# Performance work log

Measured on AMD Instinct MI355X. Metric: run time of the kernel, lower is better.

## Reference

```python
import jax, jax.numpy as jnp
import numpy as np

N_ITEMS = 7000
N_USERS = 30000
N_NODES = N_ITEMS + N_USERS  # 37000
D = 128        # embed_dim == user_embed_dim
E = 400000     # num edges
R = 10         # n_relation (num ratings)
NB = 8         # num_bases
B = 512        # batch of conversations
L = 100        # max context items per sample


def setup_inputs() -> dict:
    key = jax.random.key(0)
    ks = jax.random.split(key, 16)
    # edges: item (source) -> user (target), disjoint id ranges as in load_data
    src = jax.random.randint(ks[0], (E,), 0, N_ITEMS)
    dst = jax.random.randint(ks[1], (E,), N_ITEMS, N_NODES)
    edge_index = jnp.stack([src, dst]).astype(jnp.int64)
    edge_type = jax.random.randint(ks[2], (E,), 0, R).astype(jnp.int64)

    def make_ctx(k1, k2):
        c = jax.random.randint(k1, (B, L), 0, N_ITEMS)
        drop = jax.random.uniform(k2, (B, L)) < 0.3  # -1 padding as in batch lists
        return jnp.where(drop, -1, c).astype(jnp.int64)

    ctx_init = make_ctx(ks[3], ks[4])
    ctx_resp = make_ctx(ks[5], ks[6])

    s = 0.02
    basis = jax.random.normal(ks[7], (NB, N_NODES, D), jnp.float32) * s
    comp = jax.random.normal(ks[8], (R, NB), jnp.float32) * s
    root = jax.random.normal(ks[9], (N_NODES, D), jnp.float32) * s
    bias = jnp.zeros((D,), jnp.float32)
    attn_a = jax.random.normal(ks[10], (D, D), jnp.float32) * s
    attn_b = jax.random.normal(ks[11], (D,), jnp.float32) * s
    fc1_w = jax.random.normal(ks[12], (D, D), jnp.float32) * s
    fc1_b = jnp.zeros((D,), jnp.float32)
    fc2_w = jax.random.normal(ks[13], (D, D), jnp.float32) * s
    fc2_b = jnp.zeros((D,), jnp.float32)
    efc1_w = jax.random.normal(ks[14], (2 * D, D), jnp.float32) * s
    efc1_b = jnp.zeros((D,), jnp.float32)
    efc2_w = jax.random.normal(ks[15], (D, D), jnp.float32) * s
    efc2_b = jnp.zeros((D,), jnp.float32)
    return dict(edge_index=edge_index, edge_type=edge_type, ctx_init=ctx_init,
                ctx_resp=ctx_resp, basis=basis, comp=comp, root=root, bias=bias,
                attn_a=attn_a, attn_b=attn_b, fc1_w=fc1_w, fc1_b=fc1_b,
                fc2_w=fc2_w, fc2_b=fc2_b, efc1_w=efc1_w, efc1_b=efc1_b,
                efc2_w=efc2_w, efc2_b=efc2_b)


def _rgcn(basis, comp, root, bias, edge_index, edge_type):
    # RGCNConv with x=None: per-edge message W_{r_e}[src_e], mean-aggregated
    # per (target, relation), summed over relations, plus root lookup + bias.
    src, dst = edge_index[0], edge_index[1]
    nb, n, d = basis.shape
    r = comp.shape[0]
    cpe = comp[edge_type]  # [E, NB]
    msg = jnp.zeros((src.shape[0], d), basis.dtype)
    for b in range(nb):  # small fixed basis count; avoids [E,NB,D] gather
        msg = msg + cpe[:, b:b + 1] * basis[b][src]
    seg = dst * r + edge_type  # per-(node, relation) segment for mean aggr
    sums = jax.ops.segment_sum(msg, seg, num_segments=n * r).reshape(n, r, d)
    cnt = jax.ops.segment_sum(jnp.ones_like(edge_type, basis.dtype), seg,
                              num_segments=n * r).reshape(n, r, 1)
    return root + bias + (sums / jnp.maximum(cnt, 1.0)).sum(axis=1)  # [N, D]


def _item_user_means(node_emb, edge_index):
    # mean over users connected to each item (edge_idx[1][edge_idx[0]==item])
    src, dst = edge_index[0], edge_index[1]
    isum = jax.ops.segment_sum(node_emb[dst], src, num_segments=N_ITEMS)
    icnt = jax.ops.segment_sum(jnp.ones_like(src, node_emb.dtype), src,
                               num_segments=N_ITEMS)
    item_mean = isum / jnp.maximum(icnt, 1.0)[:, None]  # [N_ITEMS, D]
    return item_mean, icnt > 0


def _attn_pool(ctx, item_mean, item_has_users, attn_a, attn_b):
    # SelfAttentionBatch over each sample's item reps (padding/-1 & degree-0
    # items masked out; all-empty samples -> zeros, as in original).
    valid = ctx >= 0
    idx = jnp.clip(ctx, 0, N_ITEMS - 1)
    h = item_mean[idx]                       # [B, L, D]
    valid = valid & item_has_users[idx]
    e = jnp.einsum('bld,d->bl', jnp.tanh(jnp.einsum('bld,de->ble', h, attn_a)),
                   attn_b)
    attn = jax.nn.softmax(jnp.where(valid, e, -1e9), axis=-1)
    attn = jnp.where(valid, attn, 0.0)
    return jnp.einsum('bl,bld->bd', attn, h)  # [B, D]


def _project(x, w1, b1, w2, b2):
    # fc1 -> relu -> fc2 -> relu (as in _project_user_interaction_*)
    return jax.nn.relu(jax.nn.relu(x @ w1 + b1) @ w2 + b2)


def reference(edge_index, edge_type, ctx_init, ctx_resp, basis, comp, root,
              bias, attn_a, attn_b, fc1_w, fc1_b, fc2_w, fc2_b, efc1_w,
              efc1_b, efc2_w, efc2_b):
    node_emb = _rgcn(basis, comp, root, bias, edge_index, edge_type)
    item_mean, item_has = _item_user_means(node_emb, edge_index)
    p_init = _project(_attn_pool(ctx_init, item_mean, item_has, attn_a, attn_b),
                      fc1_w, fc1_b, fc2_w, fc2_b)
    p_resp = _project(_attn_pool(ctx_resp, item_mean, item_has, attn_a, attn_b),
                      fc1_w, fc1_b, fc2_w, fc2_b)
    both = jnp.concatenate([p_init, p_resp], axis=1)  # [B, 2D]
    profile = _project(both, efc1_w, efc1_b, efc2_w, efc2_b)  # [B, D]
    return profile, p_init, p_resp
```

## Files before the change

### kernel.cpp

```cpp
#include <hip/hip_runtime.h>
#include <math.h>

typedef unsigned int uint;

#define N_ITEMS 7000
#define N_NODES 37000
#define N_USERS 30000
#define DIM     128
#define HD      64
#define NREL    10
#define NBASES  8
#define BATCH   512
#define CTXL    100
#define E_MAX   400000

#define OFF_CNT    0
#define OFF_ICNT   (OFF_CNT + N_USERS * NREL)
#define OFF_UCNT   (OFF_ICNT + N_ITEMS)
#define ZERO_ELEMS (OFF_UCNT + N_USERS)
#define OFF_ICUR   ZERO_ELEMS
#define OFF_UCUR   (OFF_ICUR + N_ITEMS)
#define OFF_ICSR   (OFF_UCUR + N_USERS)
#define OFF_UCSR   (OFF_ICSR + E_MAX)
#define OFF_WC     (OFF_UCSR + E_MAX)
#define OFF_ACC    (OFF_WC + NREL * N_ITEMS * HD)
#define OFF_MEAN   (OFF_ACC + N_USERS * HD)
#define OFF_SCORE  (OFF_MEAN + N_ITEMS * HD)

__device__ __forceinline__ float2 bf2f(uint p) {
  float2 r;
  r.x = __uint_as_float(p << 16);
  r.y = __uint_as_float(p & 0xffff0000u);
  return r;
}
__device__ __forceinline__ uint f2bf(float x, float y) {
  uint a = __float_as_uint(x), b = __float_as_uint(y);
  a += 0x7fffu + ((a >> 16) & 1u);
  b += 0x7fffu + ((b >> 16) & 1u);
  return (a >> 16) | (b & 0xffff0000u);
}

__device__ __forceinline__ float wave_sum(float v) {
#pragma unroll
  for (int o = 1; o < 64; o <<= 1) v += __shfl_xor(v, o, 64);
  return v;
}
__device__ __forceinline__ float wave_max(float v) {
#pragma unroll
  for (int o = 1; o < 64; o <<= 1) v = fmaxf(v, __shfl_xor(v, o, 64));
  return v;
}

__global__ __launch_bounds__(HD) void k_combine(const float* __restrict__ basis,
                                                const float* __restrict__ comp,
                                                uint* __restrict__ Wc) {
  int i = blockIdx.x, t = threadIdx.x;
  float2 bb[NBASES];
#pragma unroll
  for (int b = 0; b < NBASES; ++b)
    bb[b] = ((const float2*)(basis + ((size_t)b * N_NODES + i) * DIM))[t];
#pragma unroll
  for (int r = 0; r < NREL; ++r) {
    float sx = 0.f, sy = 0.f;
#pragma unroll
    for (int b = 0; b < NBASES; ++b) {
      float c = comp[r * NBASES + b];
      sx = fmaf(c, bb[b].x, sx);
      sy = fmaf(c, bb[b].y, sy);
    }
    Wc[((size_t)r * N_ITEMS + i) * HD + t] = f2bf(sx, sy);
  }
}

__global__ __launch_bounds__(256) void k_count(const int* __restrict__ ei,
                                               const int* __restrict__ et, int E,
                                               int* __restrict__ cnt,
                                               int* __restrict__ icnt,
                                               int* __restrict__ ucnt) {
  int e = blockIdx.x * 256 + threadIdx.x;
  if (e >= E) return;
  int s = ei[e];
  int u0 = ei[E + e] - N_ITEMS;
  int t = et[e];
  atomicAdd(&cnt[u0 * NREL + t], 1);
  atomicAdd(&icnt[s], 1);
  atomicAdd(&ucnt[u0], 1);
}

__global__ __launch_bounds__(1024) void k_scan(const int* __restrict__ icnt,
                                               const int* __restrict__ ucnt,
                                               int* __restrict__ icur,
                                               int* __restrict__ ucur) {
  __shared__ int ss[1024];
  const int* in;
  int n;
  int* cur;
  if (blockIdx.x == 0) { in = icnt; n = N_ITEMS; cur = icur; }
  else                 { in = ucnt; n = N_USERS; cur = ucur; }
  int t = threadIdx.x;
  int chunk = (n + 1023) / 1024;
  int lo = t * chunk, hi = lo + chunk;
  if (lo > n) lo = n;
  if (hi > n) hi = n;
  int s = 0;
  for (int i = lo; i < hi; ++i) s += in[i];
  ss[t] = s;
  __syncthreads();
  for (int o = 1; o < 1024; o <<= 1) {
    int v = (t >= o) ? ss[t - o] : 0;
    __syncthreads();
    ss[t] += v;
    __syncthreads();
  }
  int base = (t > 0) ? ss[t - 1] : 0;
  for (int i = lo; i < hi; ++i) { cur[i] = base; base += in[i]; }
}

__global__ __launch_bounds__(256) void k_fill(const int* __restrict__ ei,
                                              const int* __restrict__ et, int E,
                                              int* __restrict__ icur,
                                              int* __restrict__ ucur,
                                              int* __restrict__ icsr,
                                              int* __restrict__ ucsr) {
  int e = blockIdx.x * 256 + threadIdx.x;
  if (e >= E) return;
  int s = ei[e];
  int u0 = ei[E + e] - N_ITEMS;
  int t = et[e];
  icsr[atomicAdd(&icur[s], 1)] = u0;
  ucsr[atomicAdd(&ucur[u0], 1)] = s | (t << 16);
}

__global__ __launch_bounds__(HD) void k_useragg(const int* __restrict__ ucnt,
                                                const int* __restrict__ ucur,
                                                const int* __restrict__ ucsr,
                                                const int* __restrict__ cnt,
                                                const uint* __restrict__ Wc,
                                                const float* __restrict__ root,
                                                uint* __restrict__ acc) {
  __shared__ float wrow[NREL];
  __shared__ int sedge[HD];
  int u = blockIdx.x, t = threadIdx.x;
  if (t < NREL) {
    int c = cnt[u * NREL + t];
    wrow[t] = (c > 0) ? 1.0f / (float)c : 0.0f;
  }
  int deg = ucnt[u];
  int base = ucur[u] - deg;
  float2 a0 = {0.f, 0.f}, a1 = {0.f, 0.f}, a2 = {0.f, 0.f}, a3 = {0.f, 0.f};
  for (int j0 = 0; j0 < deg; j0 += HD) {
    int m = deg - j0;
    if (m > HD) m = HD;
    __syncthreads();
    if (t < m) sedge[t] = ucsr[base + j0 + t];
    __syncthreads();
    int j = 0;
    for (; j + 4 <= m; j += 4) {
      int p0 = sedge[j], p1 = sedge[j + 1], p2 = sedge[j + 2], p3 = sedge[j + 3];
      uint q0 = Wc[(size_t)((p0 >> 16) * N_ITEMS + (p0 & 0xffff)) * HD + t];
      uint q1 = Wc[(size_t)((p1 >> 16) * N_ITEMS + (p1 & 0xffff)) * HD + t];
      uint q2 = Wc[(size_t)((p2 >> 16) * N_ITEMS + (p2 & 0xffff)) * HD + t];
      uint q3 = Wc[(size_t)((p3 >> 16) * N_ITEMS + (p3 & 0xffff)) * HD + t];
      float w0 = wrow[p0 >> 16], w1 = wrow[p1 >> 16];
      float w2 = wrow[p2 >> 16], w3 = wrow[p3 >> 16];
      float2 f0 = bf2f(q0), f1 = bf2f(q1), f2 = bf2f(q2), f3 = bf2f(q3);
      a0.x = fmaf(w0, f0.x, a0.x); a0.y = fmaf(w0, f0.y, a0.y);
      a1.x = fmaf(w1, f1.x, a1.x); a1.y = fmaf(w1, f1.y, a1.y);
      a2.x = fmaf(w2, f2.x, a2.x); a2.y = fmaf(w2, f2.y, a2.y);
      a3.x = fmaf(w3, f3.x, a3.x); a3.y = fmaf(w3, f3.y, a3.y);
    }
    for (; j < m; ++j) {
      int p = sedge[j];
      uint q = Wc[(size_t)((p >> 16) * N_ITEMS + (p & 0xffff)) * HD + t];
      float w = wrow[p >> 16];
      float2 f = bf2f(q);
      a0.x = fmaf(w, f.x, a0.x); a0.y = fmaf(w, f.y, a0.y);
    }
  }
  float2 r = ((const float2*)(root + (size_t)(N_ITEMS + u) * DIM))[t];
  r.x += a0.x + a1.x + a2.x + a3.x;
  r.y += a0.y + a1.y + a2.y + a3.y;
  acc[(size_t)u * HD + t] = f2bf(r.x, r.y);
}

__global__ __launch_bounds__(HD) void k_itemagg(const int* __restrict__ icnt,
                                                const int* __restrict__ icur,
                                                const int* __restrict__ icsr,
                                                const uint* __restrict__ acc,
                                                const float* __restrict__ bias,
                                                const float* __restrict__ attn_a,
                                                const float* __restrict__ attn_b,
                                                uint* __restrict__ mean,
                                                float* __restrict__ score) {
  __shared__ int sedge[HD];
  __shared__ float sm[DIM];
  int i = blockIdx.x, t = threadIdx.x;
  int deg = icnt[i];
  int base = icur[i] - deg;
  float2 a0 = {0.f, 0.f}, a1 = {0.f, 0.f}, a2 = {0.f, 0.f}, a3 = {0.f, 0.f};
  for (int j0 = 0; j0 < deg; j0 += HD) {
    int m = deg - j0;
    if (m > HD) m = HD;
    __syncthreads();
    if (t < m) sedge[t] = icsr[base + j0 + t];
    __syncthreads();
    int j = 0;
    for (; j + 4 <= m; j += 4) {
      uint q0 = acc[(size_t)sedge[j] * HD + t];
      uint q1 = acc[(size_t)sedge[j + 1] * HD + t];
      uint q2 = acc[(size_t)sedge[j + 2] * HD + t];
      uint q3 = acc[(size_t)sedge[j + 3] * HD + t];
      float2 f0 = bf2f(q0), f1 = bf2f(q1), f2 = bf2f(q2), f3 = bf2f(q3);
      a0.x += f0.x; a0.y += f0.y;
      a1.x += f1.x; a1.y += f1.y;
      a2.x += f2.x; a2.y += f2.y;
      a3.x += f3.x; a3.y += f3.y;
    }
    for (; j < m; ++j) {
      float2 f = bf2f(acc[(size_t)sedge[j] * HD + t]);
      a0.x += f.x; a0.y += f.y;
    }
  }
  float2 mv = {0.f, 0.f};
  if (deg > 0) {
    float inv = 1.0f / (float)deg;
    float2 bvec = ((const float2*)bias)[t];
    mv.x = (a0.x + a1.x + a2.x + a3.x) * inv + bvec.x;
    mv.y = (a0.y + a1.y + a2.y + a3.y) * inv + bvec.y;
  }
  mean[(size_t)i * HD + t] = f2bf(mv.x, mv.y);
  sm[2 * t] = mv.x;
  sm[2 * t + 1] = mv.y;
  __syncthreads();
  float z0 = 0.f, z1 = 0.f;
#pragma unroll 8
  for (int k = 0; k < DIM; ++k) {
    float2 w = ((const float2*)(attn_a + (size_t)k * DIM))[t];
    float h = sm[k];
    z0 = fmaf(h, w.x, z0);
    z1 = fmaf(h, w.y, z1);
  }
  float2 ab = ((const float2*)attn_b)[t];
  float v = wave_sum(tanhf(z0) * ab.x + tanhf(z1) * ab.y);
  if (t == 0) score[i] = (deg > 0) ? v : -1e9f;
}

__global__ __launch_bounds__(HD) void k_pool(const int* __restrict__ ctx0,
                                             const int* __restrict__ ctx1,
                                             const uint* __restrict__ mean,
                                             const float* __restrict__ score,
                                             const float* __restrict__ fc1_w,
                                             const float* __restrict__ fc1_b,
                                             const float* __restrict__ fc2_w,
                                             const float* __restrict__ fc2_b,
                                             float* __restrict__ out) {
  __shared__ float shw[CTXL];
  __shared__ int shi[CTXL];
  __shared__ float shv[DIM];
  int b = blockIdx.x & (BATCH - 1);
  int c = blockIdx.x >> 9;
  int t = threadIdx.x;
  const int* cx = (c == 0 ? ctx0 : ctx1) + (size_t)b * CTXL;

  int id0 = cx[t];
  float e0 = (id0 >= 0) ? score[id0] : -1e9f;
  int id1 = -1;
  float e1 = -3.0e38f;
  if (t + HD < CTXL) {
    id1 = cx[t + HD];
    e1 = (id1 >= 0) ? score[id1] : -1e9f;
  }
  float m = wave_max(fmaxf(e0, e1));
  float x0 = expf(e0 - m);
  float x1 = (t + HD < CTXL) ? expf(e1 - m) : 0.f;
  float inv = 1.0f / wave_sum(x0 + x1);
  shw[t] = (id0 >= 0) ? x0 * inv : 0.f;
  shi[t] = (id0 >= 0) ? id0 : 0;
  if (t + HD < CTXL) {
    shw[t + HD] = (id1 >= 0) ? x1 * inv : 0.f;
    shi[t + HD] = (id1 >= 0) ? id1 : 0;
  }
  __syncthreads();

  float2 a0 = {0.f, 0.f}, a1 = {0.f, 0.f}, a2 = {0.f, 0.f}, a3 = {0.f, 0.f};
#pragma unroll 5
  for (int l = 0; l < CTXL; l += 4) {
    float w0 = shw[l], w1 = shw[l + 1], w2 = shw[l + 2], w3 = shw[l + 3];
    uint q0 = mean[(size_t)shi[l] * HD + t];
    uint q1 = mean[(size_t)shi[l + 1] * HD + t];
    uint q2 = mean[(size_t)shi[l + 2] * HD + t];
    uint q3 = mean[(size_t)shi[l + 3] * HD + t];
    float2 f0 = bf2f(q0), f1 = bf2f(q1), f2 = bf2f(q2), f3 = bf2f(q3);
    a0.x = fmaf(w0, f0.x, a0.x); a0.y = fmaf(w0, f0.y, a0.y);
    a1.x = fmaf(w1, f1.x, a1.x); a1.y = fmaf(w1, f1.y, a1.y);
    a2.x = fmaf(w2, f2.x, a2.x); a2.y = fmaf(w2, f2.y, a2.y);
    a3.x = fmaf(w3, f3.x, a3.x); a3.y = fmaf(w3, f3.y, a3.y);
  }
  __syncthreads();
  shv[2 * t] = a0.x + a1.x + a2.x + a3.x;
  shv[2 * t + 1] = a0.y + a1.y + a2.y + a3.y;
  __syncthreads();

  float2 z = ((const float2*)fc1_b)[t];
#pragma unroll 8
  for (int k = 0; k < DIM; ++k) {
    float2 w = ((const float2*)(fc1_w + (size_t)k * DIM))[t];
    float h = shv[k];
    z.x = fmaf(h, w.x, z.x);
    z.y = fmaf(h, w.y, z.y);
  }
  z.x = fmaxf(z.x, 0.f);
  z.y = fmaxf(z.y, 0.f);
  __syncthreads();
  shv[2 * t] = z.x;
  shv[2 * t + 1] = z.y;
  __syncthreads();

  float2 z2 = ((const float2*)fc2_b)[t];
#pragma unroll 8
  for (int k = 0; k < DIM; ++k) {
    float2 w = ((const float2*)(fc2_w + (size_t)k * DIM))[t];
    float h = shv[k];
    z2.x = fmaf(h, w.x, z2.x);
    z2.y = fmaf(h, w.y, z2.y);
  }
  z2.x = fmaxf(z2.x, 0.f);
  z2.y = fmaxf(z2.y, 0.f);
  ((float2*)(out + (size_t)(1 + c) * BATCH * DIM + (size_t)b * DIM))[t] = z2;
}

__global__ __launch_bounds__(HD) void k_profile(const float* __restrict__ efc1_w,
                                                const float* __restrict__ efc1_b,
                                                const float* __restrict__ efc2_w,
                                                const float* __restrict__ efc2_b,
                                                float* __restrict__ out) {
  __shared__ float shv[2 * DIM];
  __shared__ float sh2[DIM];
  int b = blockIdx.x, t = threadIdx.x;
  float2 p0 = ((const float2*)(out + (size_t)BATCH * DIM + (size_t)b * DIM))[t];
  float2 p1 = ((const float2*)(out + (size_t)2 * BATCH * DIM + (size_t)b * DIM))[t];
  shv[2 * t] = p0.x;
  shv[2 * t + 1] = p0.y;
  shv[DIM + 2 * t] = p1.x;
  shv[DIM + 2 * t + 1] = p1.y;
  __syncthreads();
  float2 z = ((const float2*)efc1_b)[t];
#pragma unroll 8
  for (int k = 0; k < 2 * DIM; ++k) {
    float2 w = ((const float2*)(efc1_w + (size_t)k * DIM))[t];
    float h = shv[k];
    z.x = fmaf(h, w.x, z.x);
    z.y = fmaf(h, w.y, z.y);
  }
  z.x = fmaxf(z.x, 0.f);
  z.y = fmaxf(z.y, 0.f);
  __syncthreads();
  sh2[2 * t] = z.x;
  sh2[2 * t + 1] = z.y;
  __syncthreads();
  float2 z2 = ((const float2*)efc2_b)[t];
#pragma unroll 8
  for (int k = 0; k < DIM; ++k) {
    float2 w = ((const float2*)(efc2_w + (size_t)k * DIM))[t];
    float h = sh2[k];
    z2.x = fmaf(h, w.x, z2.x);
    z2.y = fmaf(h, w.y, z2.y);
  }
  z2.x = fmaxf(z2.x, 0.f);
  z2.y = fmaxf(z2.y, 0.f);
  ((float2*)(out + (size_t)b * DIM))[t] = z2;
}

extern "C" void kernel_launch(void* const* d_in, const int* in_sizes, int n_in,
                              void* d_out, int out_size, void* d_ws, size_t ws_size,
                              hipStream_t stream) {
  const int*   ei     = (const int*)d_in[0];
  const int*   et     = (const int*)d_in[1];
  const int*   ctx0   = (const int*)d_in[2];
  const int*   ctx1   = (const int*)d_in[3];
  const float* basis  = (const float*)d_in[4];
  const float* comp   = (const float*)d_in[5];
  const float* root   = (const float*)d_in[6];
  const float* bias   = (const float*)d_in[7];
  const float* attn_a = (const float*)d_in[8];
  const float* attn_b = (const float*)d_in[9];
  const float* fc1_w  = (const float*)d_in[10];
  const float* fc1_b  = (const float*)d_in[11];
  const float* fc2_w  = (const float*)d_in[12];
  const float* fc2_b  = (const float*)d_in[13];
  const float* efc1_w = (const float*)d_in[14];
  const float* efc1_b = (const float*)d_in[15];
  const float* efc2_w = (const float*)d_in[16];
  const float* efc2_b = (const float*)d_in[17];
  float* out = (float*)d_out;

  const int E = in_sizes[1];

  float* ws   = (float*)d_ws;
  int*  cnt   = (int*)(ws + OFF_CNT);
  int*  icnt  = (int*)(ws + OFF_ICNT);
  int*  ucnt  = (int*)(ws + OFF_UCNT);
  int*  icur  = (int*)(ws + OFF_ICUR);
  int*  ucur  = (int*)(ws + OFF_UCUR);
  int*  icsr  = (int*)(ws + OFF_ICSR);
  int*  ucsr  = (int*)(ws + OFF_UCSR);
  uint* Wc    = (uint*)(ws + OFF_WC);
  uint* acc   = (uint*)(ws + OFF_ACC);
  uint* mean  = (uint*)(ws + OFF_MEAN);
  float* score = ws + OFF_SCORE;

  hipMemsetAsync(d_ws, 0, (size_t)ZERO_ELEMS * sizeof(float), stream);

  k_combine<<<N_ITEMS, HD, 0, stream>>>(basis, comp, Wc);
  k_count<<<(E + 255) / 256, 256, 0, stream>>>(ei, et, E, cnt, icnt, ucnt);
  k_scan<<<2, 1024, 0, stream>>>(icnt, ucnt, icur, ucur);
  k_fill<<<(E + 255) / 256, 256, 0, stream>>>(ei, et, E, icur, ucur, icsr, ucsr);
  k_useragg<<<N_USERS, HD, 0, stream>>>(ucnt, ucur, ucsr, cnt, Wc, root, acc);
  k_itemagg<<<N_ITEMS, HD, 0, stream>>>(icnt, icur, icsr, acc, bias, attn_a, attn_b,
                                        mean, score);
  k_pool<<<2 * BATCH, HD, 0, stream>>>(ctx0, ctx1, mean, score, fc1_w, fc1_b,
                                       fc2_w, fc2_b, out);
  k_profile<<<BATCH, HD, 0, stream>>>(efc1_w, efc1_b, efc2_w, efc2_b, out);
}
```

Baseline: 481.3 us.

## Fuse combine/count and pool/profile kernels, use wave shuffles instead of LDS

Merges the basis-combine and edge-count kernels into one launch, and the pooling and profile kernels into one 128-thread block per batch row. The user and item aggregation kernels now broadcast edge indices and relation weights through wave shuffles instead of shared memory with barriers. They also unroll 16 gathers per step into 8 accumulators to keep more loads in flight. This cuts launch count, barriers and LDS traffic, at the cost of more registers and some gathers that are issued and then masked out on partial chunks.

```diff
diff --git a/kernel.cpp b/kernel.cpp
--- a/kernel.cpp
+++ b/kernel.cpp
@@ -51,40 +51,45 @@
   return v;
 }
 
-__global__ __launch_bounds__(HD) void k_combine(const float* __restrict__ basis,
-                                                const float* __restrict__ comp,
-                                                uint* __restrict__ Wc) {
-  int i = blockIdx.x, t = threadIdx.x;
-  float2 bb[NBASES];
-#pragma unroll
-  for (int b = 0; b < NBASES; ++b)
-    bb[b] = ((const float2*)(basis + ((size_t)b * N_NODES + i) * DIM))[t];
-#pragma unroll
-  for (int r = 0; r < NREL; ++r) {
-    float sx = 0.f, sy = 0.f;
-#pragma unroll
-    for (int b = 0; b < NBASES; ++b) {
-      float c = comp[r * NBASES + b];
-      sx = fmaf(c, bb[b].x, sx);
-      sy = fmaf(c, bb[b].y, sy);
-    }
-    Wc[((size_t)r * N_ITEMS + i) * HD + t] = f2bf(sx, sy);
-  }
-}
-
-__global__ __launch_bounds__(256) void k_count(const int* __restrict__ ei,
-                                               const int* __restrict__ et, int E,
-                                               int* __restrict__ cnt,
-                                               int* __restrict__ icnt,
-                                               int* __restrict__ ucnt) {
-  int e = blockIdx.x * 256 + threadIdx.x;
-  if (e >= E) return;
-  int s = ei[e];
-  int u0 = ei[E + e] - N_ITEMS;
-  int t = et[e];
-  atomicAdd(&cnt[u0 * NREL + t], 1);
-  atomicAdd(&icnt[s], 1);
-  atomicAdd(&ucnt[u0], 1);
+#define COMBINE_BLOCKS (N_ITEMS / 4)
+__global__ __launch_bounds__(256) void k_initcomb(const float* __restrict__ basis,
+                                                  const float* __restrict__ comp,
+                                                  uint* __restrict__ Wc,
+                                                  const int* __restrict__ ei,
+                                                  const int* __restrict__ et, int E,
+                                                  int* __restrict__ cnt,
+                                                  int* __restrict__ icnt,
+                                                  int* __restrict__ ucnt) {
+  int tid = threadIdx.x;
+  if (blockIdx.x < COMBINE_BLOCKS) {
+    int i = blockIdx.x * 4 + (tid >> 6);
+    int lane = tid & 63;
+    float2 bb[NBASES];
+#pragma unroll
+    for (int b = 0; b < NBASES; ++b)
+      bb[b] = ((const float2*)basis)[((size_t)b * N_NODES + i) * HD + lane];
+#pragma unroll
+    for (int r = 0; r < NREL; ++r) {
+      float sx = 0.f, sy = 0.f;
+#pragma unroll
+      for (int b = 0; b < NBASES; ++b) {
+        float c = comp[r * NBASES + b];
+        sx = fmaf(c, bb[b].x, sx);
+        sy = fmaf(c, bb[b].y, sy);
+      }
+      Wc[((size_t)r * N_ITEMS + i) * HD + lane] = f2bf(sx, sy);
+    }
+  } else {
+    int e = (blockIdx.x - COMBINE_BLOCKS) * 256 + tid;
+    if (e < E) {
+      int s  = ei[e];
+      int u0 = ei[E + e] - N_ITEMS;
+      int t  = et[e];
+      atomicAdd(&cnt[u0 * NREL + t], 1);
+      atomicAdd(&icnt[s], 1);
+      atomicAdd(&ucnt[u0], 1);
+    }
+  }
 }
 
 __global__ __launch_bounds__(1024) void k_scan(const int* __restrict__ icnt,
@@ -131,59 +136,51 @@
   ucsr[atomicAdd(&ucur[u0], 1)] = s | (t << 16);
 }
 
-__global__ __launch_bounds__(HD) void k_useragg(const int* __restrict__ ucnt,
+__global__ __launch_bounds__(64) void k_useragg(const int* __restrict__ ucnt,
                                                 const int* __restrict__ ucur,
                                                 const int* __restrict__ ucsr,
                                                 const int* __restrict__ cnt,
                                                 const uint* __restrict__ Wc,
                                                 const float* __restrict__ root,
                                                 uint* __restrict__ acc) {
-  __shared__ float wrow[NREL];
-  __shared__ int sedge[HD];
-  int u = blockIdx.x, t = threadIdx.x;
-  if (t < NREL) {
-    int c = cnt[u * NREL + t];
-    wrow[t] = (c > 0) ? 1.0f / (float)c : 0.0f;
-  }
+  int u = blockIdx.x, lane = threadIdx.x;
   int deg = ucnt[u];
   int base = ucur[u] - deg;
-  float2 a0 = {0.f, 0.f}, a1 = {0.f, 0.f}, a2 = {0.f, 0.f}, a3 = {0.f, 0.f};
-  for (int j0 = 0; j0 < deg; j0 += HD) {
+  float wl = 0.f;
+  if (lane < NREL) {
+    int c = cnt[u * NREL + lane];
+    wl = (c > 0) ? 1.0f / (float)c : 0.0f;
+  }
+  float2 av[8];
+#pragma unroll
+  for (int k = 0; k < 8; ++k) { av[k].x = 0.f; av[k].y = 0.f; }
+  for (int j0 = 0; j0 < deg; j0 += 64) {
     int m = deg - j0;
-    if (m > HD) m = HD;
-    __syncthreads();
-    if (t < m) sedge[t] = ucsr[base + j0 + t];
-    __syncthreads();
-    int j = 0;
-    for (; j + 4 <= m; j += 4) {
-      int p0 = sedge[j], p1 = sedge[j + 1], p2 = sedge[j + 2], p3 = sedge[j + 3];
-      uint q0 = Wc[(size_t)((p0 >> 16) * N_ITEMS + (p0 & 0xffff)) * HD + t];
-      uint q1 = Wc[(size_t)((p1 >> 16) * N_ITEMS + (p1 & 0xffff)) * HD + t];
-      uint q2 = Wc[(size_t)((p2 >> 16) * N_ITEMS + (p2 & 0xffff)) * HD + t];
-      uint q3 = Wc[(size_t)((p3 >> 16) * N_ITEMS + (p3 & 0xffff)) * HD + t];
-      float w0 = wrow[p0 >> 16], w1 = wrow[p1 >> 16];
-      float w2 = wrow[p2 >> 16], w3 = wrow[p3 >> 16];
-      float2 f0 = bf2f(q0), f1 = bf2f(q1), f2 = bf2f(q2), f3 = bf2f(q3);
-      a0.x = fmaf(w0, f0.x, a0.x); a0.y = fmaf(w0, f0.y, a0.y);
-      a1.x = fmaf(w1, f1.x, a1.x); a1.y = fmaf(w1, f1.y, a1.y);
-      a2.x = fmaf(w2, f2.x, a2.x); a2.y = fmaf(w2, f2.y, a2.y);
-      a3.x = fmaf(w3, f3.x, a3.x); a3.y = fmaf(w3, f3.y, a3.y);
-    }
-    for (; j < m; ++j) {
-      int p = sedge[j];
-      uint q = Wc[(size_t)((p >> 16) * N_ITEMS + (p & 0xffff)) * HD + t];
-      float w = wrow[p >> 16];
-      float2 f = bf2f(q);
-      a0.x = fmaf(w, f.x, a0.x); a0.y = fmaf(w, f.y, a0.y);
-    }
-  }
-  float2 r = ((const float2*)(root + (size_t)(N_ITEMS + u) * DIM))[t];
-  r.x += a0.x + a1.x + a2.x + a3.x;
-  r.y += a0.y + a1.y + a2.y + a3.y;
-  acc[(size_t)u * HD + t] = f2bf(r.x, r.y);
-}
-
-__global__ __launch_bounds__(HD) void k_itemagg(const int* __restrict__ icnt,
+    if (m > 64) m = 64;
+    int pl = (lane < m) ? ucsr[base + j0 + lane] : 0;
+    for (int kk = 0; kk < m; kk += 16) {
+#pragma unroll
+      for (int k = 0; k < 16; ++k) {
+        int idx = kk + k;
+        int p = __shfl(pl, idx & 63);
+        int r = p >> 16;
+        float w = (idx < m) ? __shfl(wl, r) : 0.f;
+        uint q = Wc[(size_t)(r * N_ITEMS + (p & 0xffff)) * HD + lane];
+        float2 f = bf2f(q);
+        av[k & 7].x = fmaf(w, f.x, av[k & 7].x);
+        av[k & 7].y = fmaf(w, f.y, av[k & 7].y);
+      }
+    }
+  }
+  float2 rt = ((const float2*)root)[(size_t)(N_ITEMS + u) * HD + lane];
+  rt.x += ((av[0].x + av[1].x) + (av[2].x + av[3].x)) +
+          ((av[4].x + av[5].x) + (av[6].x + av[7].x));
+  rt.y += ((av[0].y + av[1].y) + (av[2].y + av[3].y)) +
+          ((av[4].y + av[5].y) + (av[6].y + av[7].y));
+  acc[(size_t)u * HD + lane] = f2bf(rt.x, rt.y);
+}
+
+__global__ __launch_bounds__(64) void k_itemagg(const int* __restrict__ icnt,
                                                 const int* __restrict__ icur,
                                                 const int* __restrict__ icsr,
                                                 const uint* __restrict__ acc,
@@ -192,183 +189,189 @@
                                                 const float* __restrict__ attn_b,
                                                 uint* __restrict__ mean,
                                                 float* __restrict__ score) {
-  __shared__ int sedge[HD];
-  __shared__ float sm[DIM];
-  int i = blockIdx.x, t = threadIdx.x;
+  int i = blockIdx.x, lane = threadIdx.x;
   int deg = icnt[i];
   int base = icur[i] - deg;
-  float2 a0 = {0.f, 0.f}, a1 = {0.f, 0.f}, a2 = {0.f, 0.f}, a3 = {0.f, 0.f};
-  for (int j0 = 0; j0 < deg; j0 += HD) {
+  float2 av[8];
+#pragma unroll
+  for (int k = 0; k < 8; ++k) { av[k].x = 0.f; av[k].y = 0.f; }
+  for (int j0 = 0; j0 < deg; j0 += 64) {
     int m = deg - j0;
-    if (m > HD) m = HD;
-    __syncthreads();
-    if (t < m) sedge[t] = icsr[base + j0 + t];
-    __syncthreads();
-    int j = 0;
-    for (; j + 4 <= m; j += 4) {
-      uint q0 = acc[(size_t)sedge[j] * HD + t];
-      uint q1 = acc[(size_t)sedge[j + 1] * HD + t];
-      uint q2 = acc[(size_t)sedge[j + 2] * HD + t];
-      uint q3 = acc[(size_t)sedge[j + 3] * HD + t];
-      float2 f0 = bf2f(q0), f1 = bf2f(q1), f2 = bf2f(q2), f3 = bf2f(q3);
-      a0.x += f0.x; a0.y += f0.y;
-      a1.x += f1.x; a1.y += f1.y;
-      a2.x += f2.x; a2.y += f2.y;
-      a3.x += f3.x; a3.y += f3.y;
-    }
-    for (; j < m; ++j) {
-      float2 f = bf2f(acc[(size_t)sedge[j] * HD + t]);
-      a0.x += f.x; a0.y += f.y;
-    }
-  }
+    if (m > 64) m = 64;
+    int pl = (lane < m) ? icsr[base + j0 + lane] : 0;
+    for (int kk = 0; kk < m; kk += 16) {
+#pragma unroll
+      for (int k = 0; k < 16; ++k) {
+        int idx = kk + k;
+        int u0 = __shfl(pl, idx & 63);
+        uint q = acc[(size_t)u0 * HD + lane];
+        float2 f = bf2f(q);
+        if (idx < m) {
+          av[k & 7].x += f.x;
+          av[k & 7].y += f.y;
+        }
+      }
+    }
+  }
+  float sx = ((av[0].x + av[1].x) + (av[2].x + av[3].x)) +
+             ((av[4].x + av[5].x) + (av[6].x + av[7].x));
+  float sy = ((av[0].y + av[1].y) + (av[2].y + av[3].y)) +
+             ((av[4].y + av[5].y) + (av[6].y + av[7].y));
   float2 mv = {0.f, 0.f};
   if (deg > 0) {
     float inv = 1.0f / (float)deg;
-    float2 bvec = ((const float2*)bias)[t];
-    mv.x = (a0.x + a1.x + a2.x + a3.x) * inv + bvec.x;
-    mv.y = (a0.y + a1.y + a2.y + a3.y) * inv + bvec.y;
-  }
-  mean[(size_t)i * HD + t] = f2bf(mv.x, mv.y);
-  sm[2 * t] = mv.x;
-  sm[2 * t + 1] = mv.y;
-  __syncthreads();
+    float2 bv = ((const float2*)bias)[lane];
+    mv.x = sx * inv + bv.x;
+    mv.y = sy * inv + bv.y;
+  }
+  mean[(size_t)i * HD + lane] = f2bf(mv.x, mv.y);
   float z0 = 0.f, z1 = 0.f;
 #pragma unroll 8
-  for (int k = 0; k < DIM; ++k) {
-    float2 w = ((const float2*)(attn_a + (size_t)k * DIM))[t];
-    float h = sm[k];
-    z0 = fmaf(h, w.x, z0);
-    z1 = fmaf(h, w.y, z1);
-  }
-  float2 ab = ((const float2*)attn_b)[t];
+  for (int k2 = 0; k2 < HD; ++k2) {
+    float hx = __shfl(mv.x, k2);
+    float hy = __shfl(mv.y, k2);
+    float2 w0 = ((const float2*)attn_a)[(size_t)(2 * k2) * HD + lane];
+    float2 w1 = ((const float2*)attn_a)[(size_t)(2 * k2 + 1) * HD + lane];
+    z0 = fmaf(hx, w0.x, z0); z1 = fmaf(hx, w0.y, z1);
+    z0 = fmaf(hy, w1.x, z0); z1 = fmaf(hy, w1.y, z1);
+  }
+  float2 ab = ((const float2*)attn_b)[lane];
   float v = wave_sum(tanhf(z0) * ab.x + tanhf(z1) * ab.y);
-  if (t == 0) score[i] = (deg > 0) ? v : -1e9f;
-}
-
-__global__ __launch_bounds__(HD) void k_pool(const int* __restrict__ ctx0,
-                                             const int* __restrict__ ctx1,
-                                             const uint* __restrict__ mean,
-                                             const float* __restrict__ score,
-                                             const float* __restrict__ fc1_w,
-                                             const float* __restrict__ fc1_b,
-                                             const float* __restrict__ fc2_w,
-                                             const float* __restrict__ fc2_b,
-                                             float* __restrict__ out) {
-  __shared__ float shw[CTXL];
-  __shared__ int shi[CTXL];
-  __shared__ float shv[DIM];
-  int b = blockIdx.x & (BATCH - 1);
-  int c = blockIdx.x >> 9;
-  int t = threadIdx.x;
-  const int* cx = (c == 0 ? ctx0 : ctx1) + (size_t)b * CTXL;
-
-  int id0 = cx[t];
-  float e0 = (id0 >= 0) ? score[id0] : -1e9f;
-  int id1 = -1;
-  float e1 = -3.0e38f;
-  if (t + HD < CTXL) {
-    id1 = cx[t + HD];
-    e1 = (id1 >= 0) ? score[id1] : -1e9f;
-  }
-  float m = wave_max(fmaxf(e0, e1));
-  float x0 = expf(e0 - m);
-  float x1 = (t + HD < CTXL) ? expf(e1 - m) : 0.f;
-  float inv = 1.0f / wave_sum(x0 + x1);
-  shw[t] = (id0 >= 0) ? x0 * inv : 0.f;
-  shi[t] = (id0 >= 0) ? id0 : 0;
-  if (t + HD < CTXL) {
-    shw[t + HD] = (id1 >= 0) ? x1 * inv : 0.f;
-    shi[t + HD] = (id1 >= 0) ? id1 : 0;
-  }
-  __syncthreads();
-
-  float2 a0 = {0.f, 0.f}, a1 = {0.f, 0.f}, a2 = {0.f, 0.f}, a3 = {0.f, 0.f};
-#pragma unroll 5
-  for (int l = 0; l < CTXL; l += 4) {
-    float w0 = shw[l], w1 = shw[l + 1], w2 = shw[l + 2], w3 = shw[l + 3];
-    uint q0 = mean[(size_t)shi[l] * HD + t];
-    uint q1 = mean[(size_t)shi[l + 1] * HD + t];
-    uint q2 = mean[(size_t)shi[l + 2] * HD + t];
-    uint q3 = mean[(size_t)shi[l + 3] * HD + t];
-    float2 f0 = bf2f(q0), f1 = bf2f(q1), f2 = bf2f(q2), f3 = bf2f(q3);
-    a0.x = fmaf(w0, f0.x, a0.x); a0.y = fmaf(w0, f0.y, a0.y);
-    a1.x = fmaf(w1, f1.x, a1.x); a1.y = fmaf(w1, f1.y, a1.y);
-    a2.x = fmaf(w2, f2.x, a2.x); a2.y = fmaf(w2, f2.y, a2.y);
-    a3.x = fmaf(w3, f3.x, a3.x); a3.y = fmaf(w3, f3.y, a3.y);
-  }
-  __syncthreads();
-  shv[2 * t] = a0.x + a1.x + a2.x + a3.x;
-  shv[2 * t + 1] = a0.y + a1.y + a2.y + a3.y;
-  __syncthreads();
-
-  float2 z = ((const float2*)fc1_b)[t];
-#pragma unroll 8
-  for (int k = 0; k < DIM; ++k) {
-    float2 w = ((const float2*)(fc1_w + (size_t)k * DIM))[t];
-    float h = shv[k];
-    z.x = fmaf(h, w.x, z.x);
-    z.y = fmaf(h, w.y, z.y);
-  }
-  z.x = fmaxf(z.x, 0.f);
-  z.y = fmaxf(z.y, 0.f);
-  __syncthreads();
-  shv[2 * t] = z.x;
-  shv[2 * t + 1] = z.y;
-  __syncthreads();
-
-  float2 z2 = ((const float2*)fc2_b)[t];
-#pragma unroll 8
-  for (int k = 0; k < DIM; ++k) {
-    float2 w = ((const float2*)(fc2_w + (size_t)k * DIM))[t];
-    float h = shv[k];
-    z2.x = fmaf(h, w.x, z2.x);
-    z2.y = fmaf(h, w.y, z2.y);
-  }
-  z2.x = fmaxf(z2.x, 0.f);
-  z2.y = fmaxf(z2.y, 0.f);
-  ((float2*)(out + (size_t)(1 + c) * BATCH * DIM + (size_t)b * DIM))[t] = z2;
-}
-
-__global__ __launch_bounds__(HD) void k_profile(const float* __restrict__ efc1_w,
+  if (lane == 0) score[i] = (deg > 0) ? v : -1e9f;
+}
+
+__global__ __launch_bounds__(128) void k_batch2(const int* __restrict__ ctx0,
+                                                const int* __restrict__ ctx1,
+                                                const uint* __restrict__ mean,
+                                                const float* __restrict__ score,
+                                                const float* __restrict__ fc1_w,
+                                                const float* __restrict__ fc1_b,
+                                                const float* __restrict__ fc2_w,
+                                                const float* __restrict__ fc2_b,
+                                                const float* __restrict__ efc1_w,
                                                 const float* __restrict__ efc1_b,
                                                 const float* __restrict__ efc2_w,
                                                 const float* __restrict__ efc2_b,
                                                 float* __restrict__ out) {
-  __shared__ float shv[2 * DIM];
-  __shared__ float sh2[DIM];
-  int b = blockIdx.x, t = threadIdx.x;
-  float2 p0 = ((const float2*)(out + (size_t)BATCH * DIM + (size_t)b * DIM))[t];
-  float2 p1 = ((const float2*)(out + (size_t)2 * BATCH * DIM + (size_t)b * DIM))[t];
-  shv[2 * t] = p0.x;
-  shv[2 * t + 1] = p0.y;
-  shv[DIM + 2 * t] = p1.x;
-  shv[DIM + 2 * t + 1] = p1.y;
-  __syncthreads();
-  float2 z = ((const float2*)efc1_b)[t];
-#pragma unroll 8
-  for (int k = 0; k < 2 * DIM; ++k) {
-    float2 w = ((const float2*)(efc1_w + (size_t)k * DIM))[t];
-    float h = shv[k];
-    z.x = fmaf(h, w.x, z.x);
-    z.y = fmaf(h, w.y, z.y);
+  __shared__ float2 shp[2][HD];
+  int b = blockIdx.x;
+  int wv = threadIdx.x >> 6;
+  int lane = threadIdx.x & 63;
+  float2* out2 = (float2*)out;
+
+  const int* cx = (wv ? ctx1 : ctx0) + (size_t)b * CTXL;
+  int id0 = cx[lane];
+  float e0 = (id0 >= 0) ? score[id0] : -1e9f;
+  int id1 = -1;
+  float e1 = -3.0e38f;
+  if (lane < CTXL - 64) {
+    id1 = cx[64 + lane];
+    e1 = (id1 >= 0) ? score[id1] : -1e9f;
+  }
+  float mx = wave_max(fmaxf(e0, e1));
+  float x0 = expf(e0 - mx);
+  float x1 = (lane < CTXL - 64) ? expf(e1 - mx) : 0.f;
+  float inv = 1.0f / wave_sum(x0 + x1);
+  float w0 = (id0 >= 0) ? x0 * inv : 0.f;
+  float w1 = (id1 >= 0) ? x1 * inv : 0.f;
+  int i0 = (id0 >= 0) ? id0 : 0;
+  int i1 = (id1 >= 0) ? id1 : 0;
+
+  float2 av[4];
+#pragma unroll
+  for (int k = 0; k < 4; ++k) { av[k].x = 0.f; av[k].y = 0.f; }
+  for (int j = 0; j < 64; j += 4) {
+#pragma unroll
+    for (int k = 0; k < 4; ++k) {
+      int ii = __shfl(i0, j + k);
+      float ww = __shfl(w0, j + k);
+      float2 f = bf2f(mean[(size_t)ii * HD + lane]);
+      av[k].x = fmaf(ww, f.x, av[k].x);
+      av[k].y = fmaf(ww, f.y, av[k].y);
+    }
+  }
+  for (int j = 0; j < CTXL - 64; j += 4) {
+#pragma unroll
+    for (int k = 0; k < 4; ++k) {
+      int ii = __shfl(i1, j + k);
+      float ww = __shfl(w1, j + k);
+      float2 f = bf2f(mean[(size_t)ii * HD + lane]);
+      av[k].x = fmaf(ww, f.x, av[k].x);
+      av[k].y = fmaf(ww, f.y, av[k].y);
+    }
+  }
+  float2 pool;
+  pool.x = (av[0].x + av[1].x) + (av[2].x + av[3].x);
+  pool.y = (av[0].y + av[1].y) + (av[2].y + av[3].y);
+
+  float2 z = ((const float2*)fc1_b)[lane];
+#pragma unroll 8
+  for (int k2 = 0; k2 < HD; ++k2) {
+    float hx = __shfl(pool.x, k2);
+    float hy = __shfl(pool.y, k2);
+    float2 wa = ((const float2*)fc1_w)[(size_t)(2 * k2) * HD + lane];
+    float2 wb = ((const float2*)fc1_w)[(size_t)(2 * k2 + 1) * HD + lane];
+    z.x = fmaf(hx, wa.x, z.x); z.y = fmaf(hx, wa.y, z.y);
+    z.x = fmaf(hy, wb.x, z.x); z.y = fmaf(hy, wb.y, z.y);
   }
   z.x = fmaxf(z.x, 0.f);
   z.y = fmaxf(z.y, 0.f);
-  __syncthreads();
-  sh2[2 * t] = z.x;
-  sh2[2 * t + 1] = z.y;
-  __syncthreads();
-  float2 z2 = ((const float2*)efc2_b)[t];
-#pragma unroll 8
-  for (int k = 0; k < DIM; ++k) {
-    float2 w = ((const float2*)(efc2_w + (size_t)k * DIM))[t];
-    float h = sh2[k];
-    z2.x = fmaf(h, w.x, z2.x);
-    z2.y = fmaf(h, w.y, z2.y);
+
+  float2 z2 = ((const float2*)fc2_b)[lane];
+#pragma unroll 8
+  for (int k2 = 0; k2 < HD; ++k2) {
+    float hx = __shfl(z.x, k2);
+    float hy = __shfl(z.y, k2);
+    float2 wa = ((const float2*)fc2_w)[(size_t)(2 * k2) * HD + lane];
+    float2 wb = ((const float2*)fc2_w)[(size_t)(2 * k2 + 1) * HD + lane];
+    z2.x = fmaf(hx, wa.x, z2.x); z2.y = fmaf(hx, wa.y, z2.y);
+    z2.x = fmaf(hy, wb.x, z2.x); z2.y = fmaf(hy, wb.y, z2.y);
   }
   z2.x = fmaxf(z2.x, 0.f);
   z2.y = fmaxf(z2.y, 0.f);
-  ((float2*)(out + (size_t)b * DIM))[t] = z2;
+  out2[((size_t)(1 + wv) * BATCH + b) * HD + lane] = z2;
+  shp[wv][lane] = z2;
+  __syncthreads();
+
+  if (wv == 0) {
+    float2 p0 = shp[0][lane];
+    float2 p1 = shp[1][lane];
+    float2 zz = ((const float2*)efc1_b)[lane];
+#pragma unroll 8
+    for (int k2 = 0; k2 < HD; ++k2) {
+      float hx = __shfl(p0.x, k2);
+      float hy = __shfl(p0.y, k2);
+      float2 wa = ((const float2*)efc1_w)[(size_t)(2 * k2) * HD + lane];
+      float2 wb = ((const float2*)efc1_w)[(size_t)(2 * k2 + 1) * HD + lane];
+      zz.x = fmaf(hx, wa.x, zz.x); zz.y = fmaf(hx, wa.y, zz.y);
+      zz.x = fmaf(hy, wb.x, zz.x); zz.y = fmaf(hy, wb.y, zz.y);
+    }
+#pragma unroll 8
+    for (int k2 = 0; k2 < HD; ++k2) {
+      float hx = __shfl(p1.x, k2);
+      float hy = __shfl(p1.y, k2);
+      float2 wa = ((const float2*)efc1_w)[(size_t)(DIM + 2 * k2) * HD + lane];
+      float2 wb = ((const float2*)efc1_w)[(size_t)(DIM + 2 * k2 + 1) * HD + lane];
+      zz.x = fmaf(hx, wa.x, zz.x); zz.y = fmaf(hx, wa.y, zz.y);
+      zz.x = fmaf(hy, wb.x, zz.x); zz.y = fmaf(hy, wb.y, zz.y);
+    }
+    zz.x = fmaxf(zz.x, 0.f);
+    zz.y = fmaxf(zz.y, 0.f);
+
+    float2 zf = ((const float2*)efc2_b)[lane];
+#pragma unroll 8
+    for (int k2 = 0; k2 < HD; ++k2) {
+      float hx = __shfl(zz.x, k2);
+      float hy = __shfl(zz.y, k2);
+      float2 wa = ((const float2*)efc2_w)[(size_t)(2 * k2) * HD + lane];
+      float2 wb = ((const float2*)efc2_w)[(size_t)(2 * k2 + 1) * HD + lane];
+      zf.x = fmaf(hx, wa.x, zf.x); zf.y = fmaf(hx, wa.y, zf.y);
+      zf.x = fmaf(hy, wb.x, zf.x); zf.y = fmaf(hy, wb.y, zf.y);
+    }
+    zf.x = fmaxf(zf.x, 0.f);
+    zf.y = fmaxf(zf.y, 0.f);
+    out2[(size_t)b * HD + lane] = zf;
+  }
 }
 
 extern "C" void kernel_launch(void* const* d_in, const int* in_sizes, int n_in,
@@ -411,14 +414,15 @@
 
   hipMemsetAsync(d_ws, 0, (size_t)ZERO_ELEMS * sizeof(float), stream);
 
-  k_combine<<<N_ITEMS, HD, 0, stream>>>(basis, comp, Wc);
-  k_count<<<(E + 255) / 256, 256, 0, stream>>>(ei, et, E, cnt, icnt, ucnt);
+  int countBlocks = (E + 255) / 256;
+  k_initcomb<<<COMBINE_BLOCKS + countBlocks, 256, 0, stream>>>(
+      basis, comp, Wc, ei, et, E, cnt, icnt, ucnt);
   k_scan<<<2, 1024, 0, stream>>>(icnt, ucnt, icur, ucur);
-  k_fill<<<(E + 255) / 256, 256, 0, stream>>>(ei, et, E, icur, ucur, icsr, ucsr);
-  k_useragg<<<N_USERS, HD, 0, stream>>>(ucnt, ucur, ucsr, cnt, Wc, root, acc);
-  k_itemagg<<<N_ITEMS, HD, 0, stream>>>(icnt, icur, icsr, acc, bias, attn_a, attn_b,
-                                        mean, score);
-  k_pool<<<2 * BATCH, HD, 0, stream>>>(ctx0, ctx1, mean, score, fc1_w, fc1_b,
-                                       fc2_w, fc2_b, out);
-  k_profile<<<BATCH, HD, 0, stream>>>(efc1_w, efc1_b, efc2_w, efc2_b, out);
-}
+  k_fill<<<countBlocks, 256, 0, stream>>>(ei, et, E, icur, ucur, icsr, ucsr);
+  k_useragg<<<N_USERS, 64, 0, stream>>>(ucnt, ucur, ucsr, cnt, Wc, root, acc);
+  k_itemagg<<<N_ITEMS, 64, 0, stream>>>(icnt, icur, icsr, acc, bias, attn_a,
+                                        attn_b, mean, score);
+  k_batch2<<<BATCH, 128, 0, stream>>>(ctx0, ctx1, mean, score, fc1_w, fc1_b,
+                                      fc2_w, fc2_b, efc1_w, efc1_b, efc2_w,
+                                      efc2_b, out);
+}
```

Result: faster. 463.2 us (-3.8%).
